# Kernel optimization log

Measured on AMD Instinct MI355X. Metric: run time of the kernel, lower is better.

## Reference

```python
import math
import jax, jax.numpy as jnp
import numpy as np

B, T, D, CHUNK = 16, 8192, 128, 64


def setup_inputs() -> dict:
    key = jax.random.key(0)
    kq, kk, kv = jax.random.split(key, 3)
    q = jax.random.normal(kq, (B, T, D), dtype=jnp.float32)
    k = jax.random.normal(kk, (B, T, D), dtype=jnp.float32)
    v = jax.random.normal(kv, (B, T, D), dtype=jnp.float32)
    # learnable per-head decay parameter, init so sigmoid(log_decay) = 0.99
    log_decay = jnp.full((1,), math.log(0.99 / (1.0 - 0.99)), dtype=jnp.float32)
    return {"q": q, "k": k, "v": v, "log_decay": log_decay, "chunk_size": CHUNK}


def reference(q, k, v, log_decay, chunk_size):
    """Chunk-wise parallel forward of DecayedLinearState.parallel_forward.

    Returns (output [B,T,D], final_state [B,D,D], final_z [B,D]).
    """
    lam = jax.nn.sigmoid(log_decay[0])
    Bb, Tt, Dd = q.shape
    C = int(chunk_size)
    pad = (-Tt) % C
    if pad:
        q = jnp.pad(q, ((0, 0), (0, pad), (0, 0)))
        k = jnp.pad(k, ((0, 0), (0, pad), (0, 0)))
        v = jnp.pad(v, ((0, 0), (0, pad), (0, 0)))
    N = (Tt + pad) // C
    qc = q.reshape(Bb, N, C, D)  # [B,N,C,D]
    kc = k.reshape(Bb, N, C, D)
    vc = v.reshape(Bb, N, C, D)

    pos = jnp.arange(C, dtype=q.dtype)
    rel = pos[:, None] - pos[None, :]                      # i - j
    causal = jnp.tril(jnp.ones((C, C), dtype=q.dtype))
    decay_matrix = (lam ** jnp.maximum(rel, 0.0)) * causal  # [C,C]

    # intra-chunk attention for all chunks in parallel
    attn = jnp.einsum('bnic,bnjc->bnij', qc, kc) * decay_matrix  # [B,N,C,C]
    intra_out = jnp.einsum('bnij,bnjd->bnid', attn, vc)          # [B,N,C,D]
    intra_z = jnp.maximum(attn.sum(-1), 1.0)                     # [B,N,C]

    decay_q = lam ** (pos + 1.0)           # decay applied to cross-chunk reads [C]
    chunk_decay = lam ** (C - 1.0 - pos)   # decay applied to state writes     [C]
    state_decay = lam ** C

    weighted_outer = jnp.einsum('bnci,bncj,c->bnij', kc, vc, chunk_decay)  # [B,N,D,D]
    k_sum = jnp.einsum('bnci,c->bni', kc, chunk_decay)                     # [B,N,D]

    def step(carry, xs):
        state, z = carry  # [B,D,D], [B,D]
        qcn, io_n, iz_n, wo_n, ks_n = xs
        cross_out = jnp.einsum('bij,bci->bcj', state, qcn) * decay_q[None, :, None]
        cross_z = jnp.einsum('bi,bci->bc', z, qcn) * decay_q[None, :]
        total_z = jnp.maximum(iz_n + cross_z, 1.0)[..., None]
        out = (io_n + cross_out) / total_z                     # [B,C,D]
        new_state = state_decay * state + wo_n
        new_z = state_decay * z + ks_n
        return (new_state, new_z), out

    init = (jnp.zeros((Bb, D, D), q.dtype), jnp.zeros((Bb, D), q.dtype))
    xs = (qc.transpose(1, 0, 2, 3), intra_out.transpose(1, 0, 2, 3),
          intra_z.transpose(1, 0, 2), weighted_outer.transpose(1, 0, 2, 3),
          k_sum.transpose(1, 0, 2))
    (state, z), outs = jax.lax.scan(step, init, xs)  # outs: [N,B,C,D]
    output = outs.transpose(1, 0, 2, 3).reshape(Bb, N * C, D)[:, :Tt]
    return output, state, z
```

## Files before the change

### kernel.cpp

```cpp
#include <hip/hip_runtime.h>
#include <math.h>

#define Bn  16
#define Tn  8192
#define Dn  128
#define Cn  64
#define Gn  8
#define NGn 16
#define GCn 512

typedef __attribute__((ext_vector_type(8)))  short short8v;
typedef __attribute__((ext_vector_type(16))) float f32x16;

#define AK  200
#define BK  200
#define KDs 136
#define KTs 72
#define KFs 132
#define K1s 72

#define SWZ(row) ((((row) >> 2) & 7) << 3)

#define BAR() do { asm volatile("s_waitcnt lgkmcnt(0)" ::: "memory"); \
                   __builtin_amdgcn_s_barrier(); \
                   asm volatile("" ::: "memory"); } while (0)

__device__ __forceinline__ float sig_(float x){ return 1.0f/(1.0f+expf(-x)); }

__device__ __forceinline__ unsigned short f2bf(float f){
    __bf16 h = (__bf16)f;
    return __builtin_bit_cast(unsigned short, h);
}
__device__ __forceinline__ void st4(unsigned short* p, float a, float b, float c, float d){
    ushort4 u; u.x = f2bf(a); u.y = f2bf(b); u.z = f2bf(c); u.w = f2bf(d);
    *(ushort4*)p = u;
}

__global__ __launch_bounds__(512)
void k1_mfma(const float* __restrict__ kin, const float* __restrict__ vin,
             const float* __restrict__ log_decay,
             float* __restrict__ A, float* __restrict__ ksumg)
{
    const int g = blockIdx.x, b = blockIdx.y;
    const int tid  = threadIdx.x;
    const int wid  = tid >> 6;
    const int lane = tid & 63;
    const int l31  = lane & 31;
    const int lhi  = lane >> 5;
    const float lam = sig_(log_decay[0]);

    __shared__ __align__(16) unsigned short kT[128*K1s];
    __shared__ __align__(16) unsigned short vT[128*K1s];
    __shared__ float wt[GCn];
    __shared__ __align__(16) float ps[16*132];

    wt[tid] = powf(lam, (float)(GCn-1 - tid));

    const size_t base = ((size_t)b*Tn + (size_t)g*GCn)*Dn;
    const int rb = tid >> 5;
    const int cb = (tid & 31)*4;

    f32x16 acc[2];
    #pragma unroll
    for (int p = 0; p < 2; ++p)
        #pragma unroll
        for (int r = 0; r < 16; ++r) acc[p][r] = 0.f;
    float ksp[4] = {0.f, 0.f, 0.f, 0.f};

    float kv[4][4], vv[4][4];
    {
        const float* kp = kin + base;
        const float* vp = vin + base;
        #pragma unroll
        for (int u = 0; u < 4; ++u) {
            float4 t4 = *(const float4*)&kp[(size_t)(rb*4+u)*Dn + cb];
            kv[u][0]=t4.x; kv[u][1]=t4.y; kv[u][2]=t4.z; kv[u][3]=t4.w;
            float4 s4 = *(const float4*)&vp[(size_t)(rb*4+u)*Dn + cb];
            vv[u][0]=s4.x; vv[u][1]=s4.y; vv[u][2]=s4.z; vv[u][3]=s4.w;
        }
    }
    BAR();

    const int tr0 = (wid >> 2)*2;
    const int tc  = (wid & 3)*32;

    for (int t = 0; t < 8; ++t) {
        const int r0 = rb*4;
        float w0 = wt[t*64 + r0+0], w1 = wt[t*64 + r0+1];
        float w2 = wt[t*64 + r0+2], w3 = wt[t*64 + r0+3];
        #pragma unroll
        for (int e = 0; e < 4; ++e) {
            int row = cb+e, col = r0 ^ SWZ(row);
            float a0 = kv[0][e]*w0, a1 = kv[1][e]*w1, a2 = kv[2][e]*w2, a3 = kv[3][e]*w3;
            ksp[e] += (a0 + a1) + (a2 + a3);
            st4(&kT[row*K1s + col], a0, a1, a2, a3);
            st4(&vT[row*K1s + col], vv[0][e], vv[1][e], vv[2][e], vv[3][e]);
        }
        BAR();

        if (t < 7) {
            const float* kp = kin + base + (size_t)(t+1)*64*Dn;
            const float* vp = vin + base + (size_t)(t+1)*64*Dn;
            #pragma unroll
            for (int u = 0; u < 4; ++u) {
                float4 t4 = *(const float4*)&kp[(size_t)(rb*4+u)*Dn + cb];
                kv[u][0]=t4.x; kv[u][1]=t4.y; kv[u][2]=t4.z; kv[u][3]=t4.w;
                float4 s4 = *(const float4*)&vp[(size_t)(rb*4+u)*Dn + cb];
                vv[u][0]=s4.x; vv[u][1]=s4.y; vv[u][2]=s4.z; vv[u][3]=s4.w;
            }
        }

        #pragma unroll
        for (int kk = 0; kk < 4; ++kk) {
            int rB = tc + l31;
            short8v bf = *(const short8v*)&vT[rB*K1s + ((kk*16 + lhi*8) ^ SWZ(rB))];
            #pragma unroll
            for (int p = 0; p < 2; ++p) {
                int rA = (tr0+p)*32 + l31;
                short8v af = *(const short8v*)&kT[rA*K1s + ((kk*16 + lhi*8) ^ SWZ(rA))];
                acc[p] = __builtin_amdgcn_mfma_f32_32x32x16_bf16(af, bf, acc[p], 0, 0, 0);
            }
        }
        BAR();
    }

    float* Ab = A + ((size_t)(b*NGn + g))*Dn*Dn;
    #pragma unroll
    for (int p = 0; p < 2; ++p) {
        #pragma unroll
        for (int r = 0; r < 16; ++r) {
            int i = (tr0+p)*32 + (r&3) + 8*(r>>2) + 4*lhi;
            Ab[(size_t)i*Dn + tc + l31] = acc[p][r];
        }
    }

    *(float4*)&ps[rb*132 + cb] = make_float4(ksp[0], ksp[1], ksp[2], ksp[3]);
    BAR();
    if (tid < Dn) {
        float s = 0.f;
        #pragma unroll
        for (int q = 0; q < 16; ++q) s += ps[q*132 + tid];
        ksumg[((size_t)(b*NGn+g))*Dn + tid] = s;
    }
}

__global__ __launch_bounds__(256)
void k2_scan(const float* __restrict__ A, const float* __restrict__ ksumg,
             const float* __restrict__ log_decay,
             float* __restrict__ Sg, float* __restrict__ zg,
             float* __restrict__ outState, float* __restrict__ outZ)
{
    const int idx = blockIdx.x*256 + threadIdx.x;
    const float lam = sig_(log_decay[0]);
    const float dG = powf(lam, (float)GCn);
    const int NSTATE = Bn*Dn*Dn;
    if (idx < NSTATE) {
        const int b = idx >> 14, ij = idx & 16383;
        float s = 0.f;
        #pragma unroll
        for (int g = 0; g < NGn; ++g) {
            size_t o = (((size_t)(b*NGn+g)) << 14) + ij;
            Sg[o] = s;
            s = dG*s + A[o];
        }
        outState[idx] = s;
    } else if (idx < NSTATE + Bn*Dn) {
        const int j = idx - NSTATE, b = j >> 7, d = j & 127;
        float s = 0.f;
        #pragma unroll
        for (int g = 0; g < NGn; ++g) {
            size_t o = (size_t)(b*NGn+g)*Dn + d;
            zg[o] = s;
            s = dG*s + ksumg[o];
        }
        outZ[j] = s;
    }
}

__global__ __launch_bounds__(512, 2)
void k3_mfma(const float* __restrict__ qin, const float* __restrict__ kin,
             const float* __restrict__ vin, const float* __restrict__ log_decay,
             const float* __restrict__ Sg, const float* __restrict__ zg,
             float* __restrict__ out)
{
    const int g = blockIdx.x, b = blockIdx.y;
    const int tid  = threadIdx.x;
    const int wid  = tid >> 6;
    const int lane = tid & 63;
    const int l31  = lane & 31;
    const int lhi  = lane >> 5;
    const float lam   = sig_(log_decay[0]);
    const float lam64 = powf(lam, 64.0f);

    __shared__ __align__(16) unsigned short sA [64*AK];
    __shared__ __align__(16) unsigned short sB [128*BK];
    __shared__ __align__(16) unsigned short sKd[64*KDs];
    __shared__ __align__(16) unsigned short sKT[128*KTs];
    __shared__ __align__(16) float kf[64*KFs];
    __shared__ __align__(16) float zf[128];
    __shared__ __align__(16) float izb[64], czb[64];
    __shared__ float ptabs[66], ntabs[64];

    const int bg = b*NGn + g;
    const size_t base = (size_t)b*Tn + (size_t)g*Gn*Cn;

    if (tid < 66)  ptabs[tid] = powf(lam, (float)tid);
    if (tid >= 66 && tid < 130) ntabs[tid-66] = powf(lam, -(float)(tid-65));
    if (tid < 128) zf[tid] = zg[(size_t)bg*Dn + tid];

    f32x16 sacc[4];
    if (wid >= 4) {
        const float* Sgp = Sg + ((size_t)bg << 14);
        const int er0 = (wid-4)*32;
        #pragma unroll
        for (int ct = 0; ct < 4; ++ct) {
            const int d = ct*32 + l31;
            #pragma unroll
            for (int r = 0; r < 16; ++r) {
                int e = er0 + (r&3) + 8*(r>>2) + 4*lhi;
                sacc[ct][r] = Sgp[e*Dn + d];
            }
            #pragma unroll
            for (int q = 0; q < 4; ++q) {
                int e0 = er0 + 8*q + 4*lhi;
                st4(&sB[d*BK + 64 + e0],
                    sacc[ct][4*q], sacc[ct][4*q+1], sacc[ct][4*q+2], sacc[ct][4*q+3]);
            }
        }
    }

    const int a4  = (tid >> 5)*4;
    const int b4c = (tid & 31)*4;

    float qv[4][4], kv[4][4], vv[4][4];
    #pragma unroll
    for (int u = 0; u < 4; ++u) {
        float4 tq = *(const float4*)&qin[(base + a4+u)*Dn + b4c];
        qv[u][0]=tq.x; qv[u][1]=tq.y; qv[u][2]=tq.z; qv[u][3]=tq.w;
        float4 tk = *(const float4*)&kin[(base + a4+u)*Dn + b4c];
        kv[u][0]=tk.x; kv[u][1]=tk.y; kv[u][2]=tk.z; kv[u][3]=tk.w;
        float4 tv = *(const float4*)&vin[(base + a4+u)*Dn + b4c];
        vv[u][0]=tv.x; vv[u][1]=tv.y; vv[u][2]=tv.z; vv[u][3]=tv.w;
    }

    const int r0 = (wid >> 2)*32;
    const int c0 = (wid & 3)*32;

    BAR();

    for (int m = 0; m < Gn; ++m) {
        const size_t rowbase = base + (size_t)m*Cn;

        float qc[4][4];
        #pragma unroll
        for (int u = 0; u < 4; ++u) {
            const int row = a4 + u;
            const float s = ptabs[row+1];
            st4(&sA[row*AK + 64 + b4c], qv[u][0]*s, qv[u][1]*s, qv[u][2]*s, qv[u][3]*s);
            #pragma unroll
            for (int x = 0; x < 4; ++x) qc[u][x] = qv[u][x];
        }
        #pragma unroll
        for (int u = 0; u < 4; ++u)
            *(float4*)&kf[(a4+u)*KFs + b4c] = make_float4(kv[u][0],kv[u][1],kv[u][2],kv[u][3]);
        #pragma unroll
        for (int u = 0; u < 4; ++u) {
            float s = ntabs[a4+u];
            st4(&sKd[(a4+u)*KDs + b4c], kv[u][0]*s, kv[u][1]*s, kv[u][2]*s, kv[u][3]*s);
        }
        {
            float w0 = ptabs[63-a4], w1 = ptabs[62-a4], w2 = ptabs[61-a4], w3 = ptabs[60-a4];
            #pragma unroll
            for (int e = 0; e < 4; ++e) {
                int row = b4c + e, col = a4 ^ SWZ(row);
                st4(&sKT[row*KTs + col], kv[0][e]*w0, kv[1][e]*w1, kv[2][e]*w2, kv[3][e]*w3);
                st4(&sB [row*BK  + col], vv[0][e], vv[1][e], vv[2][e], vv[3][e]);
            }
        }
        if (m + 1 < Gn) {
            const size_t nrow = rowbase + Cn;
            #pragma unroll
            for (int u = 0; u < 4; ++u) {
                float4 tq = *(const float4*)&qin[(nrow + a4+u)*Dn + b4c];
                qv[u][0]=tq.x; qv[u][1]=tq.y; qv[u][2]=tq.z; qv[u][3]=tq.w;
                float4 tk = *(const float4*)&kin[(nrow + a4+u)*Dn + b4c];
                kv[u][0]=tk.x; kv[u][1]=tk.y; kv[u][2]=tk.z; kv[u][3]=tk.w;
                float4 tv = *(const float4*)&vin[(nrow + a4+u)*Dn + b4c];
                vv[u][0]=tv.x; vv[u][1]=tv.y; vv[u][2]=tv.z; vv[u][3]=tv.w;
            }
        }
        BAR();

        if (wid < 2) {
            const int d = tid;
            float kap = 0.f;
            for (int bb = 0; bb < 4; ++bb) {
                float rr[16];
                #pragma unroll
                for (int j = 0; j < 16; ++j) rr[j] = kf[(bb*16+j)*KFs + d];
                #pragma unroll
                for (int j = 0; j < 16; ++j) { kap = lam*kap + rr[j]; rr[j] = kap; }
                #pragma unroll
                for (int j = 0; j < 16; ++j) kf[(bb*16+j)*KFs + d] = rr[j];
            }
        } else if (wid < 4) {
            const int ic = (wid - 2)*32;
            #pragma unroll
            for (int jj = 0; jj < 2; ++jj) {
                const int jr = jj*32;
                f32x16 acc;
                #pragma unroll
                for (int r = 0; r < 16; ++r) acc[r] = 0.f;
                #pragma unroll
                for (int kk = 0; kk < 8; ++kk) {
                    short8v af = *(const short8v*)&sKd[(jr + l31)*KDs + kk*16 + lhi*8];
                    short8v bf = *(const short8v*)&sA [(ic + l31)*AK + 64 + kk*16 + lhi*8];
                    acc = __builtin_amdgcn_mfma_f32_32x32x16_bf16(af, bf, acc, 0, 0, 0);
                }
                const int i = ic + l31;
                #pragma unroll
                for (int q = 0; q < 4; ++q) {
                    int j0 = jr + 8*q + 4*lhi;
                    float v0 = (j0+0 <= i) ? acc[4*q+0] : 0.f;
                    float v1 = (j0+1 <= i) ? acc[4*q+1] : 0.f;
                    float v2 = (j0+2 <= i) ? acc[4*q+2] : 0.f;
                    float v3 = (j0+3 <= i) ? acc[4*q+3] : 0.f;
                    st4(&sA[i*AK + j0], v0, v1, v2, v3);
                }
            }
        } else {
            const int er0 = (wid-4)*32;
            #pragma unroll
            for (int ct = 0; ct < 4; ++ct)
                #pragma unroll
                for (int r = 0; r < 16; ++r) sacc[ct][r] *= lam64;
            #pragma unroll
            for (int kk = 0; kk < 4; ++kk) {
                int rA = er0 + l31;
                short8v af = *(const short8v*)&sKT[rA*KTs + ((kk*16 + lhi*8) ^ SWZ(rA))];
                #pragma unroll
                for (int ct = 0; ct < 4; ++ct) {
                    int rB = ct*32 + l31;
                    short8v bf = *(const short8v*)&sB[rB*BK + ((kk*16 + lhi*8) ^ SWZ(rB))];
                    sacc[ct] = __builtin_amdgcn_mfma_f32_32x32x16_bf16(af, bf, sacc[ct], 0, 0, 0);
                }
            }
        }
        BAR();

        {
            float aI[4], aZ[4];
            #pragma unroll
            for (int u = 0; u < 4; ++u) {
                const int row = a4 + u;
                float4 kp = *(const float4*)&kf[row*KFs + b4c];
                float4 zv = *(const float4*)&zf[b4c];
                aI[u] = qc[u][0]*kp.x + qc[u][1]*kp.y + qc[u][2]*kp.z + qc[u][3]*kp.w;
                aZ[u] = qc[u][0]*zv.x + qc[u][1]*zv.y + qc[u][2]*zv.z + qc[u][3]*zv.w;
            }
            #pragma unroll
            for (int u = 0; u < 4; ++u) {
                aI[u] += __shfl_xor(aI[u], 1);  aZ[u] += __shfl_xor(aZ[u], 1);
                aI[u] += __shfl_xor(aI[u], 2);  aZ[u] += __shfl_xor(aZ[u], 2);
                aI[u] += __shfl_xor(aI[u], 4);  aZ[u] += __shfl_xor(aZ[u], 4);
                aI[u] += __shfl_xor(aI[u], 8);  aZ[u] += __shfl_xor(aZ[u], 8);
                aI[u] += __shfl_xor(aI[u], 16); aZ[u] += __shfl_xor(aZ[u], 16);
            }
            if ((tid & 31) == 0) {
                #pragma unroll
                for (int u = 0; u < 4; ++u) {
                    izb[a4+u] = aI[u];
                    czb[a4+u] = ptabs[a4+u+1]*aZ[u];
                }
            }
        }
        f32x16 oacc;
        #pragma unroll
        for (int r = 0; r < 16; ++r) oacc[r] = 0.f;
        #pragma unroll
        for (int kk = 0; kk < 12; ++kk) {
            short8v af = *(const short8v*)&sA[(r0 + l31)*AK + kk*16 + lhi*8];
            int rB = c0 + l31;
            int coff = kk*16 + lhi*8;
            if (kk < 4) coff ^= SWZ(rB);
            short8v bf = *(const short8v*)&sB[rB*BK + coff];
            oacc = __builtin_amdgcn_mfma_f32_32x32x16_bf16(af, bf, oacc, 0, 0, 0);
        }
        BAR();

        #pragma unroll
        for (int r = 0; r < 16; ++r) {
            int t = r0 + (r&3) + 8*(r>>2) + 4*lhi;
            float tz = fmaxf(fmaxf(izb[t], 1.f) + czb[t], 1.f);
            out[(rowbase + t)*Dn + c0 + l31] = oacc[r] * __builtin_amdgcn_rcpf(tz);
        }
        if (wid >= 4) {
            const int er0 = (wid-4)*32;
            #pragma unroll
            for (int ct = 0; ct < 4; ++ct) {
                const int d = ct*32 + l31;
                #pragma unroll
                for (int q = 0; q < 4; ++q) {
                    int e0 = er0 + 8*q + 4*lhi;
                    st4(&sB[d*BK + 64 + e0],
                        sacc[ct][4*q], sacc[ct][4*q+1], sacc[ct][4*q+2], sacc[ct][4*q+3]);
                }
            }
        }
        if (tid < 128) {
            zf[tid] = lam64*zf[tid] + kf[63*KFs + tid];
        }
        BAR();
    }
}

extern "C" void kernel_launch(void* const* d_in, const int* in_sizes, int n_in,
                              void* d_out, int out_size, void* d_ws, size_t ws_size,
                              hipStream_t stream)
{
    const float* q  = (const float*)d_in[0];
    const float* k  = (const float*)d_in[1];
    const float* v  = (const float*)d_in[2];
    const float* ld = (const float*)d_in[3];
    float* out = (float*)d_out;

    float* A     = (float*)d_ws;
    float* ksumg = A     + (size_t)Bn*NGn*Dn*Dn;
    float* Sg    = ksumg + (size_t)Bn*NGn*Dn;
    float* zg    = Sg    + (size_t)Bn*NGn*Dn*Dn;

    float* outState = out      + (size_t)Bn*Tn*Dn;
    float* outZ     = outState + (size_t)Bn*Dn*Dn;

    hipLaunchKernelGGL(k1_mfma, dim3(NGn, Bn), dim3(512), 0, stream,
                       k, v, ld, A, ksumg);

    const int total2 = Bn*Dn*Dn + Bn*Dn;
    hipLaunchKernelGGL(k2_scan, dim3((total2 + 255)/256), dim3(256), 0, stream,
                       A, ksumg, ld, Sg, zg, outState, outZ);

    hipLaunchKernelGGL(k3_mfma, dim3(NGn, Bn), dim3(512), 0, stream,
                       q, k, v, ld, Sg, zg, out);
}
```

Measured before the change: 94.28 us.

## Prefetch MFMA operands before barrier and use DPP row reductions for normalizer sums

Loads the B operands and the part of the A operand that does not depend on the barrier into registers before the barrier. The MFMA chain is split so eight MFMAs run while the izb/czb dot-product reductions proceed. The shfl_xor butterfly reductions are replaced with DPP-based 32-lane row reductions, and the result is written from lane 16 of each half-wave. This aims to cut LDS latency stalls and the cost of cross-lane shuffles, at the price of higher register pressure, which may reduce occupancy or cause spills.

```diff
diff --git a/kernel.cpp b/kernel.cpp
--- a/kernel.cpp
+++ b/kernel.cpp
@@ -34,6 +34,20 @@
 __device__ __forceinline__ void st4(unsigned short* p, float a, float b, float c, float d){
     ushort4 u; u.x = f2bf(a); u.y = f2bf(b); u.z = f2bf(c); u.w = f2bf(d);
     *(ushort4*)p = u;
+}
+
+template<int CTRL>
+__device__ __forceinline__ float dppadd(float x){
+    int y = __builtin_amdgcn_update_dpp(0, __builtin_bit_cast(int, x), CTRL, 0xf, 0xf, true);
+    return x + __builtin_bit_cast(float, y);
+}
+__device__ __forceinline__ float red32(float x){
+    x = dppadd<0xB1>(x);
+    x = dppadd<0x4E>(x);
+    x = dppadd<0x124>(x);
+    x = dppadd<0x128>(x);
+    x = dppadd<0x142>(x);
+    return x;
 }
 
 __global__ __launch_bounds__(512)
@@ -346,46 +360,51 @@
                 }
             }
         }
-        BAR();
-
-        {
-            float aI[4], aZ[4];
-            #pragma unroll
-            for (int u = 0; u < 4; ++u) {
-                const int row = a4 + u;
-                float4 kp = *(const float4*)&kf[row*KFs + b4c];
-                float4 zv = *(const float4*)&zf[b4c];
-                aI[u] = qc[u][0]*kp.x + qc[u][1]*kp.y + qc[u][2]*kp.z + qc[u][3]*kp.w;
-                aZ[u] = qc[u][0]*zv.x + qc[u][1]*zv.y + qc[u][2]*zv.z + qc[u][3]*zv.w;
-            }
-            #pragma unroll
-            for (int u = 0; u < 4; ++u) {
-                aI[u] += __shfl_xor(aI[u], 1);  aZ[u] += __shfl_xor(aZ[u], 1);
-                aI[u] += __shfl_xor(aI[u], 2);  aZ[u] += __shfl_xor(aZ[u], 2);
-                aI[u] += __shfl_xor(aI[u], 4);  aZ[u] += __shfl_xor(aZ[u], 4);
-                aI[u] += __shfl_xor(aI[u], 8);  aZ[u] += __shfl_xor(aZ[u], 8);
-                aI[u] += __shfl_xor(aI[u], 16); aZ[u] += __shfl_xor(aZ[u], 16);
-            }
-            if ((tid & 31) == 0) {
-                #pragma unroll
-                for (int u = 0; u < 4; ++u) {
-                    izb[a4+u] = aI[u];
-                    czb[a4+u] = ptabs[a4+u+1]*aZ[u];
-                }
-            }
-        }
-        f32x16 oacc;
-        #pragma unroll
-        for (int r = 0; r < 16; ++r) oacc[r] = 0.f;
+        short8v pbf[12], paf[8];
         #pragma unroll
         for (int kk = 0; kk < 12; ++kk) {
-            short8v af = *(const short8v*)&sA[(r0 + l31)*AK + kk*16 + lhi*8];
             int rB = c0 + l31;
             int coff = kk*16 + lhi*8;
             if (kk < 4) coff ^= SWZ(rB);
-            short8v bf = *(const short8v*)&sB[rB*BK + coff];
-            oacc = __builtin_amdgcn_mfma_f32_32x32x16_bf16(af, bf, oacc, 0, 0, 0);
-        }
+            pbf[kk] = *(const short8v*)&sB[rB*BK + coff];
+        }
+        #pragma unroll
+        for (int kk = 0; kk < 8; ++kk)
+            paf[kk] = *(const short8v*)&sA[(r0 + l31)*AK + (kk+4)*16 + lhi*8];
+        BAR();
+
+        short8v afa[4];
+        #pragma unroll
+        for (int kk = 0; kk < 4; ++kk)
+            afa[kk] = *(const short8v*)&sA[(r0 + l31)*AK + kk*16 + lhi*8];
+        float aI[4], aZ[4];
+        {
+            float4 zv = *(const float4*)&zf[b4c];
+            #pragma unroll
+            for (int u = 0; u < 4; ++u) {
+                float4 kp = *(const float4*)&kf[(a4+u)*KFs + b4c];
+                aI[u] = qc[u][0]*kp.x + qc[u][1]*kp.y + qc[u][2]*kp.z + qc[u][3]*kp.w;
+                aZ[u] = qc[u][0]*zv.x + qc[u][1]*zv.y + qc[u][2]*zv.z + qc[u][3]*zv.w;
+            }
+        }
+        f32x16 oacc;
+        #pragma unroll
+        for (int r = 0; r < 16; ++r) oacc[r] = 0.f;
+        #pragma unroll
+        for (int kk = 4; kk < 12; ++kk)
+            oacc = __builtin_amdgcn_mfma_f32_32x32x16_bf16(paf[kk-4], pbf[kk], oacc, 0, 0, 0);
+        #pragma unroll
+        for (int u = 0; u < 4; ++u) { aI[u] = red32(aI[u]); aZ[u] = red32(aZ[u]); }
+        if ((lane & 31) == 16) {
+            #pragma unroll
+            for (int u = 0; u < 4; ++u) {
+                izb[a4+u] = aI[u];
+                czb[a4+u] = ptabs[a4+u+1]*aZ[u];
+            }
+        }
+        #pragma unroll
+        for (int kk = 0; kk < 4; ++kk)
+            oacc = __builtin_amdgcn_mfma_f32_32x32x16_bf16(afa[kk], pbf[kk], oacc, 0, 0, 0);
         BAR();
 
         #pragma unroll
```

After: 143.2 us. 1.52x slower.
